# Performance work log

Measured on AMD Instinct MI355X. Metric: run time of the kernel, lower is better.

The kernel has to match this reference:

```python
import jax, jax.numpy as jnp
import numpy as np

B, S, E, H, L, A, OBS = 4, 1024, 512, 8, 4, 8, 128
D_HEAD = E // H
EPS = 1e-6
DECAY_SCALING = 1.0


def rmsnorm(x, scale):
    return x * jax.lax.rsqrt(jnp.mean(x * x, -1, keepdims=True) + EPS) * scale


def swiglu_ffn(x, w_gate, w_lin, w_out):
    return (jax.nn.silu(x @ w_gate) * (x @ w_lin)) @ w_out


def retention(x, h, logk, w_q, w_k, w_v, w_g, w_o, gns, gnb, ts, seg):
    # x:[B,S,E]  h:[B,H,d,d]  ts/seg:[B,S] int  logk:[H]
    q = (x @ w_q).reshape(B, S, H, D_HEAD).transpose(0, 2, 1, 3)
    k = (x @ w_k).reshape(B, S, H, D_HEAD).transpose(0, 2, 1, 3) / jnp.sqrt(jnp.asarray(D_HEAD, x.dtype))
    v = (x @ w_v).reshape(B, S, H, D_HEAD).transpose(0, 2, 1, 3)
    dt = (ts[:, :, None] - ts[:, None, :]).astype(x.dtype)            # [B,S,S]
    mask = (dt >= 0) & (seg[:, :, None] == seg[:, None, :])           # timestep-causal, same episode
    dt = jnp.where(mask, dt, 0.0)
    Dm = jnp.where(mask[:, None], jnp.exp(dt[:, None] * logk[None, :, None, None]), 0.0)  # [B,H,S,S]
    scores = jnp.einsum('bhnd,bhmd->bhnm', q, k) * Dm
    inner = jnp.einsum('bhnm,bhme->bhne', scores, v)
    tsf = ts.astype(x.dtype)
    fresh = (seg == 0).astype(x.dtype)                                # prev-chunk state only valid pre-done
    xi = jnp.exp((tsf + 1.0)[:, None, :] * logk[None, :, None]) * fresh[:, None, :]  # [B,H,S]
    cross = jnp.einsum('bhn,bhnd,bhde->bhne', xi, q, h)
    ret = inner + cross                                               # [B,H,S,d]
    # chunk-final recurrent state
    tmax = tsf[:, -1]
    eta = jnp.exp((tmax[:, None] - tsf)[:, None, :] * logk[None, :, None])
    eta = eta * (seg == seg[:, -1:]).astype(x.dtype)[:, None, :]
    keep = (seg[:, -1] == 0).astype(x.dtype)
    h_decay = jnp.exp((tmax + 1.0)[:, None] * logk[None, :]) * keep[:, None]  # [B,H]
    h_new = h * h_decay[..., None, None] + jnp.einsum('bhm,bhmd,bhme->bhde', eta, k, v)
    # per-head group norm (num_groups = n_head)
    y = ret.transpose(0, 2, 1, 3)                                     # [B,S,H,d]
    mu = jnp.mean(y, -1, keepdims=True)
    var = jnp.mean((y - mu) ** 2, -1, keepdims=True)
    y = ((y - mu) * jax.lax.rsqrt(var + EPS)).reshape(B, S, E) * gns + gnb
    out = (jax.nn.silu(x @ w_g) * y) @ w_o
    return out, h_new


def forward(obs, hstate, dones, timestep_id, ln_enc_scale, w_enc, ln_shared,
            wq, wk, wv, wg, wo, gn_scale, gn_bias, ln1_s, ln2_s,
            sw_gate, sw_lin, sw_out, head_w1, head_b1, head_ln, head_w2, head_b2):
    kappas = (1.0 - jnp.exp(jnp.linspace(jnp.log(1.0 / 32.0), jnp.log(1.0 / 512.0), H))) * DECAY_SCALING
    logk = jnp.log(kappas).astype(obs.dtype)
    seg = jnp.cumsum(dones, axis=-1)
    x = jax.nn.gelu(rmsnorm(obs, ln_enc_scale) @ w_enc)               # obs encoder
    new_h = jnp.zeros_like(hstate)
    for i in range(L):
        xin = rmsnorm(x, ln_shared)
        ret, hn = retention(xin, hstate[:, :, i], logk, wq[i], wk[i], wv[i], wg[i], wo[i],
                            gn_scale[i], gn_bias[i], timestep_id, seg)
        x1 = rmsnorm(xin + ret, ln1_s[i])
        x = rmsnorm(x1 + swiglu_ffn(x1, sw_gate[i], sw_lin[i], sw_out[i]), ln2_s[i])
        new_h = new_h.at[:, :, i].set(hn)
    z = jax.nn.gelu(x @ head_w1 + head_b1)
    v_loc = rmsnorm(z, head_ln) @ head_w2 + head_b2
    return v_loc, x, new_h


def setup_inputs() -> dict:
    key = jax.random.key(0)
    ks = jax.random.split(key, 16)
    sc = 0.02
    f = jnp.float32
    return {
        'obs': jax.random.normal(ks[0], (B, S, OBS), f),
        'hstate': jax.random.normal(ks[1], (B, H, L, D_HEAD, D_HEAD), f) * 0.1,
        'dones': (jax.random.uniform(ks[2], (B, S)) < 0.01).astype(jnp.int32),
        'timestep_id': jnp.broadcast_to(jnp.repeat(jnp.arange(S // A, dtype=jnp.int32), A)[None], (B, S)),
        'ln_enc_scale': jnp.ones((OBS,), f),
        'w_enc': jax.random.normal(ks[3], (OBS, E), f) * sc,
        'ln_shared': jnp.ones((E,), f),
        'wq': jax.random.normal(ks[4], (L, E, E), f) * sc,
        'wk': jax.random.normal(ks[5], (L, E, E), f) * sc,
        'wv': jax.random.normal(ks[6], (L, E, E), f) * sc,
        'wg': jax.random.normal(ks[7], (L, E, E), f) * sc,
        'wo': jax.random.normal(ks[8], (L, E, E), f) * sc,
        'gn_scale': jnp.ones((L, E), f),
        'gn_bias': jnp.zeros((L, E), f),
        'ln1_s': jnp.ones((L, E), f),
        'ln2_s': jnp.ones((L, E), f),
        'sw_gate': jax.random.normal(ks[9], (L, E, E), f) * sc,
        'sw_lin': jax.random.normal(ks[10], (L, E, E), f) * sc,
        'sw_out': jax.random.normal(ks[11], (L, E, E), f) * sc,
        'head_w1': jax.random.normal(ks[12], (E, E), f) * sc,
        'head_b1': jnp.zeros((E,), f),
        'head_ln': jnp.ones((E,), f),
        'head_w2': jax.random.normal(ks[13], (E, 1), f) * 0.01,
        'head_b2': jnp.zeros((1,), f),
    }


def reference(obs, hstate, dones, timestep_id, ln_enc_scale, w_enc, ln_shared,
              wq, wk, wv, wg, wo, gn_scale, gn_bias, ln1_s, ln2_s,
              sw_gate, sw_lin, sw_out, head_w1, head_b1, head_ln, head_w2, head_b2):
    return forward(obs, hstate, dones, timestep_id, ln_enc_scale, w_enc, ln_shared,
                   wq, wk, wv, wg, wo, gn_scale, gn_bias, ln1_s, ln2_s,
                   sw_gate, sw_lin, sw_out, head_w1, head_b1, head_ln, head_w2, head_b2)
```

## Files before the change

kernel.cpp:

```cpp
#include <hip/hip_runtime.h>
#include <math.h>

#define BN 4
#define SN 1024
#define EN 512
#define HN 8
#define LN 4
#define DN 64
#define OBSN 128
#define NR (BN*SN)
#define NB (NR*EN)
#define EPSF 1e-6f

typedef __attribute__((ext_vector_type(8))) short short8v;
typedef __attribute__((ext_vector_type(4))) float f32x4;
typedef unsigned short u16;

__device__ __forceinline__ float logk_of(int h){
    const float start = -3.4657359027997265f;
    const float step  = -0.3960841031771117f;
    return logf(1.0f - expf(start + step*(float)h));
}
__device__ __forceinline__ float geluf(float x){
    float x3 = x*x*x;
    return 0.5f*x*(1.0f + tanhf(0.7978845608028654f*(x + 0.044715f*x3)));
}
__device__ __forceinline__ float siluf(float x){
    return x / (1.0f + expf(-x));
}
__device__ __forceinline__ u16 f2bf(float x){
    union { float f; unsigned u; } v; v.f = x;
    unsigned r = v.u + 0x7FFFu + ((v.u >> 16) & 1u);
    return (u16)(r >> 16);
}
__device__ __forceinline__ void load_lds16(const void* g, void* l){
    __builtin_amdgcn_global_load_lds((const __attribute__((address_space(1))) void*)g,
                                     (__attribute__((address_space(3))) void*)l, 16, 0, 0);
}
__device__ __forceinline__ int swz(int r, int bo){ return r*128 + (bo ^ ((r&7)<<4)); }

__global__ void seg_kernel(const int* __restrict__ dones, int* __restrict__ seg){
    __shared__ int sm[SN];
    int b = blockIdx.x, t = threadIdx.x;
    sm[t] = dones[b*SN + t];
    __syncthreads();
    for (int off=1; off<SN; off<<=1){
        int v = (t>=off) ? sm[t-off] : 0;
        __syncthreads();
        sm[t] += v;
        __syncthreads();
    }
    seg[b*SN + t] = sm[t];
}

__global__ void wconv8_kernel(const float* w0, const float* w1, const float* w2,
                              const float* w3, const float* w4, const float* w5,
                              const float* w6, const float* w7,
                              u16* __restrict__ dst){
    __shared__ u16 tile[32][33];
    int z = blockIdx.z;
    int type = z>>2, layer = z&3;
    const float* srcs[8] = {w0,w1,w2,w3,w4,w5,w6,w7};
    const float* s = srcs[type] + (size_t)layer*EN*EN;
    u16* d = dst + ((size_t)type*LN + layer)*EN*EN;
    int k0 = blockIdx.y*32, m0 = blockIdx.x*32;
    int tx = threadIdx.x, ty = threadIdx.y;
    #pragma unroll
    for (int i=0;i<32;i+=8)
        tile[tx][ty+i] = f2bf(s[(size_t)(k0+ty+i)*EN + m0+tx]);
    __syncthreads();
    #pragma unroll
    for (int i=0;i<32;i+=8)
        d[(size_t)(m0+ty+i)*EN + k0+tx] = tile[ty+i][tx];
}
__global__ void wconv_kernel(const float* __restrict__ src, u16* __restrict__ dst,
                             int K, int M){
    __shared__ u16 tile[32][33];
    const float* s = src;
    u16* d = dst;
    int k0 = blockIdx.y*32, m0 = blockIdx.x*32;
    int tx = threadIdx.x, ty = threadIdx.y;
    #pragma unroll
    for (int i=0;i<32;i+=8)
        tile[tx][ty+i] = f2bf(s[(size_t)(k0+ty+i)*M + m0+tx]);
    __syncthreads();
    #pragma unroll
    for (int i=0;i<32;i+=8)
        d[(size_t)(m0+ty+i)*K + k0+tx] = tile[ty+i][tx];
}

template<int COLS, bool WF32, bool WBF>
__global__ void rmsnorm_kernel(const float* __restrict__ A,
                               const float* __restrict__ scale,
                               float* __restrict__ Of,
                               u16* __restrict__ Ob){
    constexpr int PER = COLS/64;
    int row  = blockIdx.x*4 + (threadIdx.x>>6);
    int lane = threadIdx.x & 63;
    const float* a = A + (size_t)row*COLS;
    float v[PER];
    float ss = 0.f;
    #pragma unroll
    for (int i=0;i<PER;i++){
        float x = a[lane + i*64];
        v[i] = x; ss += x*x;
    }
    #pragma unroll
    for (int off=32; off>0; off>>=1) ss += __shfl_xor(ss, off, 64);
    float rs = rsqrtf(ss*(1.0f/COLS) + EPSF);
    #pragma unroll
    for (int i=0;i<PER;i++){
        float o = v[i]*rs*scale[lane + i*64];
        if (WF32) Of[(size_t)row*COLS + lane + i*64] = o;
        if (WBF)  Ob[(size_t)row*COLS + lane + i*64] = f2bf(o);
    }
}

struct TileCtx { int t, w, lane, wr, wc; };
__device__ __forceinline__ void stage_tileA(const u16* __restrict__ A, size_t rowBase,
                                            int K, int k0, u16* As, int t){
    #pragma unroll
    for (int i=0;i<2;i++){
        int o = i*4096 + t*16;
        int arow = o>>7, acolb = o&127;
        load_lds16(A + (rowBase+arow)*K + k0 + (acolb>>1), (char*)As + o);
    }
}
__device__ __forceinline__ void mma_tile(const u16* As, const u16* Bs, f32x4 acc[2][2],
                                         int wr, int wc, int lane){
    #pragma unroll
    for (int kk=0; kk<64; kk+=32){
        int kb = kk + (lane>>4)*8;
        short8v a[2], b[2];
        #pragma unroll
        for (int m=0;m<2;m++)
            a[m] = *(const short8v*)((const char*)As + (wr*32+m*16+(lane&15))*128 + kb*2);
        #pragma unroll
        for (int n=0;n<2;n++)
            b[n] = *(const short8v*)((const char*)Bs + (wc*32+n*16+(lane&15))*128 + kb*2);
        #pragma unroll
        for (int m=0;m<2;m++)
            #pragma unroll
            for (int n=0;n<2;n++)
                acc[m][n] = __builtin_amdgcn_mfma_f32_16x16x32_bf16(a[m], b[n], acc[m][n], 0,0,0);
    }
}
#define ZERO_ACC(acc) { _Pragma("unroll") for (int m=0;m<2;m++) _Pragma("unroll") for (int n=0;n<2;n++){ acc[m][n][0]=0.f;acc[m][n][1]=0.f;acc[m][n][2]=0.f;acc[m][n][3]=0.f; } }

__global__ __launch_bounds__(256) void gemm_qkvg(
    const u16* __restrict__ A,
    const u16* __restrict__ WQ, const u16* __restrict__ WK,
    const u16* __restrict__ WV, const u16* __restrict__ WG,
    u16* __restrict__ Qbb, float* __restrict__ Kb, u16* __restrict__ Kbb,
    float* __restrict__ Vb, u16* __restrict__ VtT, float* __restrict__ Gb)
{
    __shared__ u16 As[64*64];
    __shared__ u16 Bs[4][64*64];
    int t = threadIdx.x;
    int row0 = blockIdx.y*64, col0 = blockIdx.x*64;
    int w = t>>6, lane = t&63;
    int wr = w>>1, wc = w&1;
    f32x4 accQ[2][2], accK[2][2], accV[2][2], accG[2][2];
    ZERO_ACC(accQ); ZERO_ACC(accK); ZERO_ACC(accV); ZERO_ACC(accG);
    const u16* Ws[4] = {WQ, WK, WV, WG};

    for (int k0=0; k0<EN; k0+=64){
        stage_tileA(A, (size_t)row0, EN, k0, As, t);
        #pragma unroll
        for (int wt=0; wt<4; wt++){
            #pragma unroll
            for (int i=0;i<2;i++){
                int o = i*4096 + t*16;
                int brow = o>>7, bcolb = o&127;
                load_lds16(Ws[wt] + (size_t)(col0+brow)*EN + k0 + (bcolb>>1), (char*)Bs[wt] + o);
            }
        }
        __syncthreads();
        mma_tile(As, Bs[0], accQ, wr, wc, lane);
        mma_tile(As, Bs[1], accK, wr, wc, lane);
        mma_tile(As, Bs[2], accV, wr, wc, lane);
        mma_tile(As, Bs[3], accG, wr, wc, lane);
        __syncthreads();
    }
    #pragma unroll
    for (int m=0;m<2;m++){
        #pragma unroll
        for (int n=0;n<2;n++){
            int col = col0 + wc*32 + n*16 + (lane&15);
            int rbase = row0 + wr*32 + m*16 + (lane>>4)*4;
            float vv[4];
            #pragma unroll
            for (int j=0;j<4;j++){
                size_t idx = (size_t)(rbase+j)*EN + col;
                Qbb[idx] = f2bf(accQ[m][n][j]);
                float kx = accK[m][n][j]*0.125f;
                Kb[idx] = kx; Kbb[idx] = f2bf(kx);
                float vx = accV[m][n][j];
                Vb[idx] = vx; vv[j] = vx;
                Gb[idx] = siluf(accG[m][n][j]);
            }
            ushort4 pk;
            pk.x=f2bf(vv[0]); pk.y=f2bf(vv[1]); pk.z=f2bf(vv[2]); pk.w=f2bf(vv[3]);
            int bb = rbase>>10;
            int s0 = rbase&1023;
            *(ushort4*)(VtT + ((size_t)bb*EN + col)*SN + s0) = pk;
        }
    }
}

__global__ __launch_bounds__(256) void gemm_swpair(
    const u16* __restrict__ A,
    const u16* __restrict__ WGt, const u16* __restrict__ WLt,
    u16* __restrict__ Out)
{
    __shared__ u16 As[64*64];
    __shared__ u16 Bg[64*64];
    __shared__ u16 Bl[64*64];
    int t = threadIdx.x;
    int row0 = blockIdx.y*64, col0 = blockIdx.x*64;
    int w = t>>6, lane = t&63;
    int wr = w>>1, wc = w&1;
    f32x4 accG[2][2], accL[2][2];
    ZERO_ACC(accG); ZERO_ACC(accL);
    for (int k0=0; k0<EN; k0+=64){
        stage_tileA(A, (size_t)row0, EN, k0, As, t);
        #pragma unroll
        for (int i=0;i<2;i++){
            int o = i*4096 + t*16;
            int brow = o>>7, bcolb = o&127;
            load_lds16(WGt + (size_t)(col0+brow)*EN + k0 + (bcolb>>1), (char*)Bg + o);
            load_lds16(WLt + (size_t)(col0+brow)*EN + k0 + (bcolb>>1), (char*)Bl + o);
        }
        __syncthreads();
        mma_tile(As, Bg, accG, wr, wc, lane);
        mma_tile(As, Bl, accL, wr, wc, lane);
        __syncthreads();
    }
    #pragma unroll
    for (int m=0;m<2;m++){
        #pragma unroll
        for (int n=0;n<2;n++){
            int col = col0 + wc*32 + n*16 + (lane&15);
            int rbase = row0 + wr*32 + m*16 + (lane>>4)*4;
            #pragma unroll
            for (int j=0;j<4;j++){
                float x = siluf(accG[m][n][j]) * accL[m][n][j];
                Out[(size_t)(rbase+j)*EN + col] = f2bf(x);
            }
        }
    }
}

template<int ACT, bool BIASF, bool RESF, int OUTM>
__global__ __launch_bounds__(256) void gemm_bf16(
    const u16* __restrict__ A, const u16* __restrict__ Wt,
    const float* __restrict__ bias, const float* __restrict__ res,
    float* __restrict__ C, u16* __restrict__ Ob, int K, float scale)
{
    __shared__ u16 As[64*64];
    __shared__ u16 Bs[64*64];
    int t = threadIdx.x;
    int row0 = blockIdx.y*64, col0 = blockIdx.x*64;
    int w = t>>6, lane = t&63;
    int wr = w>>1, wc = w&1;
    f32x4 acc[2][2];
    ZERO_ACC(acc);
    for (int k0=0; k0<K; k0+=64){
        stage_tileA(A, (size_t)row0, K, k0, As, t);
        #pragma unroll
        for (int i=0;i<2;i++){
            int o = i*4096 + t*16;
            int brow = o>>7, bcolb = o&127;
            load_lds16(Wt + (size_t)(col0+brow)*K + k0 + (bcolb>>1), (char*)Bs + o);
        }
        __syncthreads();
        mma_tile(As, Bs, acc, wr, wc, lane);
        __syncthreads();
    }
    #pragma unroll
    for (int m=0;m<2;m++){
        #pragma unroll
        for (int n=0;n<2;n++){
            int col = col0 + wc*32 + n*16 + (lane&15);
            int rbase = row0 + wr*32 + m*16 + (lane>>4)*4;
            #pragma unroll
            for (int j=0;j<4;j++){
                float x = acc[m][n][j]*scale;
                if (BIASF) x += bias[col];
                if (ACT==1) x = siluf(x);
                if (ACT==2) x = geluf(x);
                if (RESF) x += res[(size_t)(rbase+j)*512 + col];
                if (OUTM&1) C[(size_t)(rbase+j)*512 + col] = x;
                if (OUTM&2) Ob[(size_t)(rbase+j)*512 + col] = f2bf(x);
            }
        }
    }
}

__global__ __launch_bounds__(256) void retention_mfma(
    const u16* __restrict__ Qbb, const u16* __restrict__ Kbb,
    const u16* __restrict__ VtT,
    const float* __restrict__ hstate, const int* __restrict__ tsid, const int* __restrict__ seg,
    const float* __restrict__ gns, const float* __restrict__ gnb,
    const float* __restrict__ Gb, u16* __restrict__ Out, int layer)
{
    int bh = blockIdx.y; int b = bh>>3; int h = bh&7;
    int tile = (int)gridDim.x - 1 - (int)blockIdx.x;
    int n0 = tile*64;
    int t = threadIdx.x, lane = t&63, w = t>>6;
    __shared__ u16 Qs[64*64];
    __shared__ u16 Ks[64*64];
    __shared__ u16 Vts[64*64];
    __shared__ u16 Ps[64*64];
    __shared__ float tsq_s[64], eq_s[64], xi_s[64];
    __shared__ int   segq_s[64];
    __shared__ float tsm_s[64], em_s[64];
    __shared__ int   segm_s[64];
    float lk = logk_of(h);

    #pragma unroll
    for (int i=0;i<2;i++){
        int c = t + i*256; int r = c>>3, cb = (c&7)*16;
        short8v qv = *(const short8v*)(Qbb + (size_t)(b*SN + n0 + r)*EN + h*DN + (cb>>1));
        *(short8v*)((char*)Qs + swz(r,cb)) = qv;
    }
    const float* h0 = hstate + ((size_t)bh*LN + layer)*4096;
    #pragma unroll
    for (int i=0;i<4;i++){
        int idx = t + i*256; int d = idx>>4, e0 = (idx&15)*4;
        float4 hv = *(const float4*)(h0 + d*64 + e0);
        *(u16*)((char*)Ps + swz(e0+0, 2*d)) = f2bf(hv.x);
        *(u16*)((char*)Ps + swz(e0+1, 2*d)) = f2bf(hv.y);
        *(u16*)((char*)Ps + swz(e0+2, 2*d)) = f2bf(hv.z);
        *(u16*)((char*)Ps + swz(e0+3, 2*d)) = f2bf(hv.w);
    }
    if (t<64){
        float tq = (float)tsid[b*SN+n0+t];
        int sg = seg[b*SN+n0+t];
        tsq_s[t]=tq; segq_s[t]=sg;
        eq_s[t]=expf(tq*lk);
        xi_s[t]=(sg==0)?expf((tq+1.f)*lk):0.f;
    }
    __syncthreads();

    int qlj = w*16 + ((lane>>4)<<2);
    float tsq_r[4], eq_r[4], xi_r[4]; int sgq_r[4];
    #pragma unroll
    for (int j=0;j<4;j++){
        tsq_r[j]=tsq_s[qlj+j]; eq_r[j]=eq_s[qlj+j];
        xi_r[j]=xi_s[qlj+j];  sgq_r[j]=segq_s[qlj+j];
    }
    short8v aq0 = *(short8v*)((char*)Qs + swz(w*16+(lane&15), (lane>>4)*16));
    short8v aq1 = *(short8v*)((char*)Qs + swz(w*16+(lane&15), 64 + (lane>>4)*16));

    f32x4 oacc[4];
    {
        f32x4 cacc[4];
        #pragma unroll
        for (int en=0;en<4;en++){ cacc[en][0]=0.f; cacc[en][1]=0.f; cacc[en][2]=0.f; cacc[en][3]=0.f; }
        #pragma unroll
        for (int en=0;en<4;en++){
            short8v b0 = *(short8v*)((char*)Ps + swz(en*16+(lane&15), (lane>>4)*16));
            short8v b1 = *(short8v*)((char*)Ps + swz(en*16+(lane&15), 64+(lane>>4)*16));
            cacc[en] = __builtin_amdgcn_mfma_f32_16x16x32_bf16(aq0, b0, cacc[en], 0,0,0);
            cacc[en] = __builtin_amdgcn_mfma_f32_16x16x32_bf16(aq1, b1, cacc[en], 0,0,0);
        }
        #pragma unroll
        for (int en=0;en<4;en++)
            #pragma unroll
            for (int j=0;j<4;j++) oacc[en][j] = cacc[en][j]*xi_r[j];
    }

    for (int mt=0; mt<=tile; ++mt){
        int m0 = mt*64;
        __syncthreads();
        #pragma unroll
        for (int i=0;i<2;i++){
            int c = t + i*256; int r = c>>3, cb = (c&7)*16;
            short8v kv = *(const short8v*)(Kbb + (size_t)(b*SN+m0+r)*EN + h*DN + (cb>>1));
            *(short8v*)((char*)Ks + swz(r,cb)) = kv;
            short8v vv = *(const short8v*)(VtT + ((size_t)(b*EN) + h*DN + r)*SN + m0 + (cb>>1));
            *(short8v*)((char*)Vts + swz(r,cb)) = vv;
        }
        if (t<64){
            float tm = (float)tsid[b*SN+m0+t];
            tsm_s[t]=tm; segm_s[t]=seg[b*SN+m0+t]; em_s[t]=expf(-tm*lk);
        }
        __syncthreads();
        f32x4 sacc[4];
        #pragma unroll
        for (int mn=0;mn<4;mn++){ sacc[mn][0]=0.f; sacc[mn][1]=0.f; sacc[mn][2]=0.f; sacc[mn][3]=0.f; }
        #pragma unroll
        for (int mn=0;mn<4;mn++){
            short8v b0 = *(short8v*)((char*)Ks + swz(mn*16+(lane&15), (lane>>4)*16));
            short8v b1 = *(short8v*)((char*)Ks + swz(mn*16+(lane&15), 64+(lane>>4)*16));
            sacc[mn] = __builtin_amdgcn_mfma_f32_16x16x32_bf16(aq0, b0, sacc[mn], 0,0,0);
            sacc[mn] = __builtin_amdgcn_mfma_f32_16x16x32_bf16(aq1, b1, sacc[mn], 0,0,0);
        }
        #pragma unroll
        for (int mn=0;mn<4;mn++){
            int m = mn*16 + (lane&15);
            float tm = tsm_s[m]; float em = em_s[m]; int sgm = segm_s[m];
            #pragma unroll
            for (int j=0;j<4;j++){
                float p = (tsq_r[j]>=tm && sgq_r[j]==sgm) ? sacc[mn][j]*eq_r[j]*em : 0.f;
                *(u16*)((char*)Ps + swz(qlj+j, 2*m)) = f2bf(p);
            }
        }
        short8v ap0 = *(short8v*)((char*)Ps + swz(w*16+(lane&15), (lane>>4)*16));
        short8v ap1 = *(short8v*)((char*)Ps + swz(w*16+(lane&15), 64+(lane>>4)*16));
        #pragma unroll
        for (int dn=0;dn<4;dn++){
            short8v b0 = *(short8v*)((char*)Vts + swz(dn*16+(lane&15), (lane>>4)*16));
            short8v b1 = *(short8v*)((char*)Vts + swz(dn*16+(lane&15), 64+(lane>>4)*16));
            oacc[dn] = __builtin_amdgcn_mfma_f32_16x16x32_bf16(ap0, b0, oacc[dn], 0,0,0);
            oacc[dn] = __builtin_amdgcn_mfma_f32_16x16x32_bf16(ap1, b1, oacc[dn], 0,0,0);
        }
    }

    float mu[4], rs[4];
    #pragma unroll
    for (int j=0;j<4;j++){
        float s = oacc[0][j]+oacc[1][j]+oacc[2][j]+oacc[3][j];
        #pragma unroll
        for (int off=1; off<16; off<<=1) s += __shfl_xor(s, off, 64);
        mu[j] = s*(1.0f/64.0f);
        float d0=oacc[0][j]-mu[j], d1=oacc[1][j]-mu[j], d2=oacc[2][j]-mu[j], d3=oacc[3][j]-mu[j];
        float q2 = d0*d0+d1*d1+d2*d2+d3*d3;
        #pragma unroll
        for (int off=1; off<16; off<<=1) q2 += __shfl_xor(q2, off, 64);
        rs[j] = rsqrtf(q2*(1.0f/64.0f) + EPSF);
    }
    #pragma unroll
    for (int dn=0;dn<4;dn++){
        int e = h*DN + dn*16 + (lane&15);
        float gs = gns[e], gb = gnb[e];
        #pragma unroll
        for (int j=0;j<4;j++){
            size_t row = (size_t)(b*SN + n0 + qlj + j);
            float y = (oacc[dn][j]-mu[j])*rs[j]*gs + gb;
            Out[row*EN + e] = f2bf(y * Gb[row*EN + e]);
        }
    }
}

__global__ __launch_bounds__(256) void hnew_partial(
    const float* __restrict__ Kb, const float* __restrict__ Vb,
    const int* __restrict__ tsid, const int* __restrict__ seg,
    float* __restrict__ part)
{
    int bh = blockIdx.x; int b = bh>>3; int h = bh&7;
    int ch = blockIdx.y;
    int t = threadIdx.x;
    int r = t>>4, c = t&15;
    int d = t>>2, e0 = (t&3)*16;
    __shared__ float k_s[16][68], v_s[16][68];
    __shared__ float eta_s[16];
    float lk = logk_of(h);
    float tmax = (float)tsid[b*SN + SN-1];
    int segl = seg[b*SN + SN-1];
    float acc[16] = {};
    for (int mt=ch*4; mt<ch*4+4; ++mt){
        int m0 = mt*16;
        size_t rowM = (size_t)(b*SN + m0 + r)*EN + h*64;
        *(float4*)&k_s[r][c*4] = *(const float4*)(Kb + rowM + c*4);
        *(float4*)&v_s[r][c*4] = *(const float4*)(Vb + rowM + c*4);
        if (t<16){
            float tsm = (float)tsid[b*SN+m0+t];
            eta_s[t] = (seg[b*SN+m0+t]==segl) ? expf((tmax - tsm)*lk) : 0.f;
        }
        __syncthreads();
        #pragma unroll
        for (int mm=0; mm<16; mm++){
            float ek = eta_s[mm]*k_s[mm][d];
            #pragma unroll
            for (int u=0; u<4; u++){
                float4 vv = *(float4*)&v_s[mm][e0+u*4];
                acc[u*4+0]+=ek*vv.x; acc[u*4+1]+=ek*vv.y;
                acc[u*4+2]+=ek*vv.z; acc[u*4+3]+=ek*vv.w;
            }
        }
        __syncthreads();
    }
    float* po = part + ((size_t)bh*16 + ch)*4096;
    #pragma unroll
    for (int u=0; u<4; u++)
        *(float4*)(po + d*64 + e0 + u*4) = make_float4(acc[u*4+0],acc[u*4+1],acc[u*4+2],acc[u*4+3]);
}

__global__ void hreduce_kernel(const float* __restrict__ part, const float* __restrict__ hstate,
                               const int* __restrict__ tsid, const int* __restrict__ seg,
                               float* __restrict__ Hout, int layer){
    int bh = blockIdx.x; int b = bh>>3; int h = bh&7;
    int t = threadIdx.x;
    float lk = logk_of(h);
    float tmax = (float)tsid[b*SN + SN-1];
    int segl = seg[b*SN + SN-1];
    float hd = (segl==0) ? expf((tmax+1.0f)*lk) : 0.f;
    const float* h0 = hstate + ((size_t)bh*LN + layer)*4096;
    float* ho = Hout + ((size_t)bh*LN + layer)*4096;
    int e = t*4;
    float4 s = *(const float4*)(h0 + e);
    float4 o = make_float4(s.x*hd, s.y*hd, s.z*hd, s.w*hd);
    #pragma unroll
    for (int ch=0; ch<16; ch++){
        float4 p = *(const float4*)(part + ((size_t)bh*16 + ch)*4096 + e);
        o.x+=p.x; o.y+=p.y; o.z+=p.z; o.w+=p.w;
    }
    *(float4*)(ho + e) = o;
}

__global__ void vloc_kernel(const float* __restrict__ ZN, const float* __restrict__ w2,
                            const float* __restrict__ b2, float* __restrict__ out){
    int row  = blockIdx.x*4 + (threadIdx.x>>6);
    int lane = threadIdx.x & 63;
    const float* z = ZN + (size_t)row*EN;
    float s = 0.f;
    #pragma unroll
    for (int i=0;i<8;i++) s += z[lane + i*64]*w2[lane + i*64];
    #pragma unroll
    for (int off=32; off>0; off>>=1) s += __shfl_xor(s, off, 64);
    if (lane==0) out[row] = s + b2[0];
}

static inline void launch_gemm(const u16* A, const u16* Wt, const float* bias,
                               const float* res, float* C, u16* Ob,
                               int K, float scale, int act, int outm, hipStream_t s){
    dim3 g(8, 64), b(256,1,1);
    if (bias)                    gemm_bf16<2,true ,false,1><<<g,b,0,s>>>(A,Wt,bias,res,C,Ob,K,scale);
    else if (res && outm==3)     gemm_bf16<0,false,true ,3><<<g,b,0,s>>>(A,Wt,bias,res,C,Ob,K,scale);
    else if (res)                gemm_bf16<0,false,true ,1><<<g,b,0,s>>>(A,Wt,bias,res,C,Ob,K,scale);
    else if (act==2)             gemm_bf16<2,false,false,1><<<g,b,0,s>>>(A,Wt,bias,res,C,Ob,K,scale);
    else                         gemm_bf16<0,false,false,1><<<g,b,0,s>>>(A,Wt,bias,res,C,Ob,K,scale);
}

extern "C" void kernel_launch(void* const* d_in, const int* in_sizes, int n_in,
                              void* d_out, int out_size, void* d_ws, size_t ws_size,
                              hipStream_t stream){
    const float* obs       = (const float*)d_in[0];
    const float* hstate    = (const float*)d_in[1];
    const int*   dones     = (const int*)  d_in[2];
    const int*   tsid      = (const int*)  d_in[3];
    const float* ln_enc    = (const float*)d_in[4];
    const float* w_enc     = (const float*)d_in[5];
    const float* ln_shared = (const float*)d_in[6];
    const float* wq        = (const float*)d_in[7];
    const float* wk        = (const float*)d_in[8];
    const float* wv        = (const float*)d_in[9];
    const float* wg        = (const float*)d_in[10];
    const float* wo        = (const float*)d_in[11];
    const float* gns       = (const float*)d_in[12];
    const float* gnb       = (const float*)d_in[13];
    const float* ln1       = (const float*)d_in[14];
    const float* ln2       = (const float*)d_in[15];
    const float* swg       = (const float*)d_in[16];
    const float* swl       = (const float*)d_in[17];
    const float* swo       = (const float*)d_in[18];
    const float* hw1       = (const float*)d_in[19];
    const float* hb1       = (const float*)d_in[20];
    const float* hln       = (const float*)d_in[21];
    const float* hw2       = (const float*)d_in[22];
    const float* hb2       = (const float*)d_in[23];

    float* out_v = (float*)d_out;
    float* out_x = out_v + NR;
    float* out_h = out_x + (size_t)NR*EN;

    float* ws    = (float*)d_ws;
    float* XIN   = ws + 0*(size_t)NB;
    float* Qb    = ws + 1*(size_t)NB;
    float* Kb    = ws + 2*(size_t)NB;
    float* Vb    = ws + 3*(size_t)NB;
    float* Gb    = ws + 4*(size_t)NB;
    float* Yb    = ws + 5*(size_t)NB;
    float* hpart = ws + 6*(size_t)NB;
    int*   seg   = (int*)(hpart + 32*16*4096);
    u16* wtb  = (u16*)(seg + NR);
    const size_t WEm = (size_t)EN*EN;
    u16* wqT   = wtb;
    u16* wkT   = wqT + 4*WEm;
    u16* wvT   = wkT + 4*WEm;
    u16* wgT   = wvT + 4*WEm;
    u16* woT   = wgT + 4*WEm;
    u16* sgT   = woT + 4*WEm;
    u16* slT   = sgT + 4*WEm;
    u16* soT   = slT + 4*WEm;
    u16* wencT = soT + 4*WEm;
    u16* w1T   = wencT + (size_t)EN*OBSN;
    u16* S1b   = w1T + WEm;
    u16* S2b   = S1b + (size_t)NB;
    u16* encb  = S2b + (size_t)NB;
    u16* Qbb   = encb + (size_t)NR*OBSN;
    u16* Kbb   = Qbb + (size_t)NB;
    u16* VtT   = (u16*)Qb;

    seg_kernel<<<BN, SN, 0, stream>>>(dones, seg);

    {
        dim3 tb(32,8,1);
        wconv8_kernel<<<dim3(16,16,32), tb, 0, stream>>>(wq,wk,wv,wg,wo,swg,swl,swo, wtb);
        wconv_kernel<<<dim3(16,4,1),  tb, 0, stream>>>(w_enc, wencT, OBSN, EN);
        wconv_kernel<<<dim3(16,16,1), tb, 0, stream>>>(hw1,   w1T,   EN, EN);
    }

    rmsnorm_kernel<OBSN,false,true><<<NR/4, 256, 0, stream>>>(obs, ln_enc, nullptr, encb);
    launch_gemm(encb, wencT, nullptr, nullptr, out_x, nullptr, OBSN, 1.f, 2, 1, stream);

    for (int l=0; l<LN; ++l){
        rmsnorm_kernel<EN,true,true><<<NR/4, 256, 0, stream>>>(out_x, ln_shared, XIN, S1b);
        gemm_qkvg<<<dim3(8,64), 256, 0, stream>>>(S1b,
            wqT + l*WEm, wkT + l*WEm, wvT + l*WEm, wgT + l*WEm,
            Qbb, Kb, Kbb, Vb, VtT, Gb);
        retention_mfma<<<dim3(16, BN*HN), 256, 0, stream>>>(
            Qbb, Kbb, VtT, hstate, tsid, seg, gns + l*EN, gnb + l*EN, Gb, S2b, l);
        hnew_partial<<<dim3(BN*HN, 16), 256, 0, stream>>>(Kb, Vb, tsid, seg, hpart);
        hreduce_kernel<<<BN*HN, 1024, 0, stream>>>(hpart, hstate, tsid, seg, out_h, l);
        launch_gemm(S2b, woT + l*WEm, nullptr, XIN, Qb, nullptr, EN, 1.f, 0, 1, stream);
        rmsnorm_kernel<EN,true,true><<<NR/4, 256, 0, stream>>>(Qb, ln1 + l*EN, Kb, S1b);
        gemm_swpair<<<dim3(8,64), 256, 0, stream>>>(S1b, sgT + l*WEm, slT + l*WEm, S2b);
        launch_gemm(S2b, soT + l*WEm, nullptr, Kb, Qb, nullptr, EN, 1.f, 0, 1, stream);
        if (l == LN-1)
            rmsnorm_kernel<EN,true,true ><<<NR/4, 256, 0, stream>>>(Qb, ln2 + l*EN, out_x, S1b);
        else
            rmsnorm_kernel<EN,true,false><<<NR/4, 256, 0, stream>>>(Qb, ln2 + l*EN, out_x, nullptr);
    }

    launch_gemm(S1b, w1T, hb1, nullptr, Yb, nullptr, EN, 1.f, 2, 1, stream);
    rmsnorm_kernel<EN,true,false><<<NR/4, 256, 0, stream>>>(Yb, hln, XIN, nullptr);
    vloc_kernel<<<NR/4, 256, 0, stream>>>(XIN, hw2, hb2, out_v);
}
```

Baseline: 505.4 us.

## Fuse recurrent state update into retention kernel and double-buffer GEMM tiles

The separate hnew_partial and hreduce kernels are removed. The chunk-final state is now computed by an extra block per (batch, head) inside retention_mfma, using bf16 MFMA over a transposed K copy, which cuts two launches and the fp32 K/V writes. All three GEMM kernels double-buffer their LDS tiles so the next k-slice loads while the current one computes. The retention loop register-prefetches the next K/V tile and raises wave priority around the MFMAs. In exchange, the state update now runs in bf16 instead of fp32, and the extra KtT write plus larger LDS use per GEMM block may lower occupancy.

```diff
diff --git a/kernel.cpp b/kernel.cpp
--- a/kernel.cpp
+++ b/kernel.cpp
@@ -32,6 +32,10 @@
     union { float f; unsigned u; } v; v.f = x;
     unsigned r = v.u + 0x7FFFu + ((v.u >> 16) & 1u);
     return (u16)(r >> 16);
+}
+__device__ __forceinline__ float bf2f(u16 x){
+    union { unsigned u; float f; } v; v.u = ((unsigned)x)<<16;
+    return v.f;
 }
 __device__ __forceinline__ void load_lds16(const void* g, void* l){
     __builtin_amdgcn_global_load_lds((const __attribute__((address_space(1))) void*)g,
@@ -76,17 +80,15 @@
 __global__ void wconv_kernel(const float* __restrict__ src, u16* __restrict__ dst,
                              int K, int M){
     __shared__ u16 tile[32][33];
-    const float* s = src;
-    u16* d = dst;
     int k0 = blockIdx.y*32, m0 = blockIdx.x*32;
     int tx = threadIdx.x, ty = threadIdx.y;
     #pragma unroll
     for (int i=0;i<32;i+=8)
-        tile[tx][ty+i] = f2bf(s[(size_t)(k0+ty+i)*M + m0+tx]);
+        tile[tx][ty+i] = f2bf(src[(size_t)(k0+ty+i)*M + m0+tx]);
     __syncthreads();
     #pragma unroll
     for (int i=0;i<32;i+=8)
-        d[(size_t)(m0+ty+i)*K + k0+tx] = tile[ty+i][tx];
+        dst[(size_t)(m0+ty+i)*K + k0+tx] = tile[ty+i][tx];
 }
 
 template<int COLS, bool WF32, bool WBF>
@@ -116,14 +118,13 @@
     }
 }
 
-struct TileCtx { int t, w, lane, wr, wc; };
-__device__ __forceinline__ void stage_tileA(const u16* __restrict__ A, size_t rowBase,
-                                            int K, int k0, u16* As, int t){
+__device__ __forceinline__ void stage_tile(const u16* __restrict__ G, size_t rowBase,
+                                           int K, int k0, u16* dst, int t){
     #pragma unroll
     for (int i=0;i<2;i++){
         int o = i*4096 + t*16;
-        int arow = o>>7, acolb = o&127;
-        load_lds16(A + (rowBase+arow)*K + k0 + (acolb>>1), (char*)As + o);
+        int grow = o>>7, gcolb = o&127;
+        load_lds16(G + (rowBase+grow)*K + k0 + (gcolb>>1), (char*)dst + o);
     }
 }
 __device__ __forceinline__ void mma_tile(const u16* As, const u16* Bs, f32x4 acc[2][2],
@@ -151,11 +152,11 @@
     const u16* __restrict__ A,
     const u16* __restrict__ WQ, const u16* __restrict__ WK,
     const u16* __restrict__ WV, const u16* __restrict__ WG,
-    u16* __restrict__ Qbb, float* __restrict__ Kb, u16* __restrict__ Kbb,
-    float* __restrict__ Vb, u16* __restrict__ VtT, float* __restrict__ Gb)
+    u16* __restrict__ Qbb, u16* __restrict__ Kbb,
+    u16* __restrict__ VtT, u16* __restrict__ KtT, float* __restrict__ Gb)
 {
-    __shared__ u16 As[64*64];
-    __shared__ u16 Bs[4][64*64];
+    __shared__ u16 As[2][64*64];
+    __shared__ u16 Bs[2][4][64*64];
     int t = threadIdx.x;
     int row0 = blockIdx.y*64, col0 = blockIdx.x*64;
     int w = t>>6, lane = t&63;
@@ -164,22 +165,22 @@
     ZERO_ACC(accQ); ZERO_ACC(accK); ZERO_ACC(accV); ZERO_ACC(accG);
     const u16* Ws[4] = {WQ, WK, WV, WG};
 
-    for (int k0=0; k0<EN; k0+=64){
-        stage_tileA(A, (size_t)row0, EN, k0, As, t);
-        #pragma unroll
-        for (int wt=0; wt<4; wt++){
-            #pragma unroll
-            for (int i=0;i<2;i++){
-                int o = i*4096 + t*16;
-                int brow = o>>7, bcolb = o&127;
-                load_lds16(Ws[wt] + (size_t)(col0+brow)*EN + k0 + (bcolb>>1), (char*)Bs[wt] + o);
-            }
-        }
-        __syncthreads();
-        mma_tile(As, Bs[0], accQ, wr, wc, lane);
-        mma_tile(As, Bs[1], accK, wr, wc, lane);
-        mma_tile(As, Bs[2], accV, wr, wc, lane);
-        mma_tile(As, Bs[3], accG, wr, wc, lane);
+    stage_tile(A, (size_t)row0, EN, 0, As[0], t);
+    #pragma unroll
+    for (int wt=0; wt<4; wt++) stage_tile(Ws[wt], (size_t)col0, EN, 0, Bs[0][wt], t);
+    __syncthreads();
+    for (int ti=0; ti<EN/64; ++ti){
+        int cur = ti&1;
+        if (ti+1 < EN/64){
+            stage_tile(A, (size_t)row0, EN, (ti+1)*64, As[cur^1], t);
+            #pragma unroll
+            for (int wt=0; wt<4; wt++)
+                stage_tile(Ws[wt], (size_t)col0, EN, (ti+1)*64, Bs[cur^1][wt], t);
+        }
+        mma_tile(As[cur], Bs[cur][0], accQ, wr, wc, lane);
+        mma_tile(As[cur], Bs[cur][1], accK, wr, wc, lane);
+        mma_tile(As[cur], Bs[cur][2], accV, wr, wc, lane);
+        mma_tile(As[cur], Bs[cur][3], accG, wr, wc, lane);
         __syncthreads();
     }
     #pragma unroll
@@ -188,22 +189,21 @@
         for (int n=0;n<2;n++){
             int col = col0 + wc*32 + n*16 + (lane&15);
             int rbase = row0 + wr*32 + m*16 + (lane>>4)*4;
-            float vv[4];
+            ushort4 pkV, pkK;
             #pragma unroll
             for (int j=0;j<4;j++){
                 size_t idx = (size_t)(rbase+j)*EN + col;
                 Qbb[idx] = f2bf(accQ[m][n][j]);
                 float kx = accK[m][n][j]*0.125f;
-                Kb[idx] = kx; Kbb[idx] = f2bf(kx);
-                float vx = accV[m][n][j];
-                Vb[idx] = vx; vv[j] = vx;
+                Kbb[idx] = f2bf(kx);
+                ((u16*)&pkK)[j] = f2bf(kx);
+                ((u16*)&pkV)[j] = f2bf(accV[m][n][j]);
                 Gb[idx] = siluf(accG[m][n][j]);
             }
-            ushort4 pk;
-            pk.x=f2bf(vv[0]); pk.y=f2bf(vv[1]); pk.z=f2bf(vv[2]); pk.w=f2bf(vv[3]);
             int bb = rbase>>10;
             int s0 = rbase&1023;
-            *(ushort4*)(VtT + ((size_t)bb*EN + col)*SN + s0) = pk;
+            *(ushort4*)(VtT + ((size_t)bb*EN + col)*SN + s0) = pkV;
+            *(ushort4*)(KtT + ((size_t)bb*EN + col)*SN + s0) = pkK;
         }
     }
 }
@@ -213,27 +213,28 @@
     const u16* __restrict__ WGt, const u16* __restrict__ WLt,
     u16* __restrict__ Out)
 {
-    __shared__ u16 As[64*64];
-    __shared__ u16 Bg[64*64];
-    __shared__ u16 Bl[64*64];
+    __shared__ u16 As[2][64*64];
+    __shared__ u16 Bg[2][64*64];
+    __shared__ u16 Bl[2][64*64];
     int t = threadIdx.x;
     int row0 = blockIdx.y*64, col0 = blockIdx.x*64;
     int w = t>>6, lane = t&63;
     int wr = w>>1, wc = w&1;
     f32x4 accG[2][2], accL[2][2];
     ZERO_ACC(accG); ZERO_ACC(accL);
-    for (int k0=0; k0<EN; k0+=64){
-        stage_tileA(A, (size_t)row0, EN, k0, As, t);
-        #pragma unroll
-        for (int i=0;i<2;i++){
-            int o = i*4096 + t*16;
-            int brow = o>>7, bcolb = o&127;
-            load_lds16(WGt + (size_t)(col0+brow)*EN + k0 + (bcolb>>1), (char*)Bg + o);
-            load_lds16(WLt + (size_t)(col0+brow)*EN + k0 + (bcolb>>1), (char*)Bl + o);
-        }
-        __syncthreads();
-        mma_tile(As, Bg, accG, wr, wc, lane);
-        mma_tile(As, Bl, accL, wr, wc, lane);
+    stage_tile(A, (size_t)row0, EN, 0, As[0], t);
+    stage_tile(WGt, (size_t)col0, EN, 0, Bg[0], t);
+    stage_tile(WLt, (size_t)col0, EN, 0, Bl[0], t);
+    __syncthreads();
+    for (int ti=0; ti<EN/64; ++ti){
+        int cur = ti&1;
+        if (ti+1 < EN/64){
+            stage_tile(A, (size_t)row0, EN, (ti+1)*64, As[cur^1], t);
+            stage_tile(WGt, (size_t)col0, EN, (ti+1)*64, Bg[cur^1], t);
+            stage_tile(WLt, (size_t)col0, EN, (ti+1)*64, Bl[cur^1], t);
+        }
+        mma_tile(As[cur], Bg[cur], accG, wr, wc, lane);
+        mma_tile(As[cur], Bl[cur], accL, wr, wc, lane);
         __syncthreads();
     }
     #pragma unroll
@@ -257,24 +258,25 @@
     const float* __restrict__ bias, const float* __restrict__ res,
     float* __restrict__ C, u16* __restrict__ Ob, int K, float scale)
 {
-    __shared__ u16 As[64*64];
-    __shared__ u16 Bs[64*64];
+    __shared__ u16 As[2][64*64];
+    __shared__ u16 Bs[2][64*64];
     int t = threadIdx.x;
     int row0 = blockIdx.y*64, col0 = blockIdx.x*64;
     int w = t>>6, lane = t&63;
     int wr = w>>1, wc = w&1;
     f32x4 acc[2][2];
     ZERO_ACC(acc);
-    for (int k0=0; k0<K; k0+=64){
-        stage_tileA(A, (size_t)row0, K, k0, As, t);
-        #pragma unroll
-        for (int i=0;i<2;i++){
-            int o = i*4096 + t*16;
-            int brow = o>>7, bcolb = o&127;
-            load_lds16(Wt + (size_t)(col0+brow)*K + k0 + (bcolb>>1), (char*)Bs + o);
-        }
-        __syncthreads();
-        mma_tile(As, Bs, acc, wr, wc, lane);
+    int nt = K/64;
+    stage_tile(A, (size_t)row0, K, 0, As[0], t);
+    stage_tile(Wt, (size_t)col0, K, 0, Bs[0], t);
+    __syncthreads();
+    for (int ti=0; ti<nt; ++ti){
+        int cur = ti&1;
+        if (ti+1 < nt){
+            stage_tile(A, (size_t)row0, K, (ti+1)*64, As[cur^1], t);
+            stage_tile(Wt, (size_t)col0, K, (ti+1)*64, Bs[cur^1], t);
+        }
+        mma_tile(As[cur], Bs[cur], acc, wr, wc, lane);
         __syncthreads();
     }
     #pragma unroll
@@ -299,14 +301,13 @@
 
 __global__ __launch_bounds__(256) void retention_mfma(
     const u16* __restrict__ Qbb, const u16* __restrict__ Kbb,
-    const u16* __restrict__ VtT,
+    const u16* __restrict__ VtT, const u16* __restrict__ KtT,
     const float* __restrict__ hstate, const int* __restrict__ tsid, const int* __restrict__ seg,
     const float* __restrict__ gns, const float* __restrict__ gnb,
-    const float* __restrict__ Gb, u16* __restrict__ Out, int layer)
+    const float* __restrict__ Gb, u16* __restrict__ Out,
+    float* __restrict__ Hout, int layer)
 {
     int bh = blockIdx.y; int b = bh>>3; int h = bh&7;
-    int tile = (int)gridDim.x - 1 - (int)blockIdx.x;
-    int n0 = tile*64;
     int t = threadIdx.x, lane = t&63, w = t>>6;
     __shared__ u16 Qs[64*64];
     __shared__ u16 Ks[64*64];
@@ -318,6 +319,66 @@
     __shared__ int   segm_s[64];
     float lk = logk_of(h);
 
+    if (blockIdx.x == 0){
+        float tmax = (float)tsid[b*SN + SN-1];
+        int segl = seg[b*SN + SN-1];
+        float* eta = (float*)Qs;
+        #pragma unroll
+        for (int i=0;i<4;i++){
+            int m = t + i*256;
+            float tsm = (float)tsid[b*SN+m];
+            eta[m] = (seg[b*SN+m]==segl) ? expf((tmax - tsm)*lk) : 0.f;
+        }
+        f32x4 eacc[4];
+        #pragma unroll
+        for (int en=0;en<4;en++){ eacc[en][0]=0.f; eacc[en][1]=0.f; eacc[en][2]=0.f; eacc[en][3]=0.f; }
+        for (int mt=0; mt<16; ++mt){
+            int m0 = mt*64;
+            __syncthreads();
+            #pragma unroll
+            for (int i=0;i<2;i++){
+                int c = t + i*256; int r = c>>3, cb = (c&7)*16;
+                int mb = m0 + (cb>>1);
+                size_t g = ((size_t)(b*EN) + h*DN + r)*SN + mb;
+                short8v kt = *(const short8v*)(KtT + g);
+                short8v vt = *(const short8v*)(VtT + g);
+                short8v ks;
+                #pragma unroll
+                for (int j=0;j<8;j++) ks[j] = (short)f2bf(bf2f((u16)kt[j]) * eta[mb+j]);
+                *(short8v*)((char*)Ks  + swz(r,cb)) = ks;
+                *(short8v*)((char*)Vts + swz(r,cb)) = vt;
+            }
+            __syncthreads();
+            short8v a0 = *(short8v*)((char*)Ks + swz(w*16+(lane&15), (lane>>4)*16));
+            short8v a1 = *(short8v*)((char*)Ks + swz(w*16+(lane&15), 64+(lane>>4)*16));
+            __builtin_amdgcn_s_setprio(1);
+            #pragma unroll
+            for (int en=0;en<4;en++){
+                short8v b0 = *(short8v*)((char*)Vts + swz(en*16+(lane&15), (lane>>4)*16));
+                short8v b1 = *(short8v*)((char*)Vts + swz(en*16+(lane&15), 64+(lane>>4)*16));
+                eacc[en] = __builtin_amdgcn_mfma_f32_16x16x32_bf16(a0, b0, eacc[en], 0,0,0);
+                eacc[en] = __builtin_amdgcn_mfma_f32_16x16x32_bf16(a1, b1, eacc[en], 0,0,0);
+            }
+            __builtin_amdgcn_s_setprio(0);
+        }
+        float hd = (segl==0) ? expf((tmax+1.0f)*lk) : 0.f;
+        const float* h0 = hstate + ((size_t)bh*LN + layer)*4096;
+        float* ho = Hout + ((size_t)bh*LN + layer)*4096;
+        #pragma unroll
+        for (int en=0;en<4;en++){
+            int e = en*16 + (lane&15);
+            #pragma unroll
+            for (int j=0;j<4;j++){
+                int d = w*16 + (lane>>4)*4 + j;
+                ho[d*64 + e] = h0[d*64 + e]*hd + eacc[en][j];
+            }
+        }
+        return;
+    }
+
+    int tile = 16 - (int)blockIdx.x;
+    int n0 = tile*64;
+
     #pragma unroll
     for (int i=0;i<2;i++){
         int c = t + i*256; int r = c>>3, cb = (c&7)*16;
@@ -341,6 +402,15 @@
         eq_s[t]=expf(tq*lk);
         xi_s[t]=(sg==0)?expf((tq+1.f)*lk):0.f;
     }
+    short8v kr0, kr1, vr0, vr1;
+    {
+        int c0 = t, c1 = t+256;
+        int r0=c0>>3, cb0=(c0&7)*16, r1=c1>>3, cb1=(c1&7)*16;
+        kr0 = *(const short8v*)(Kbb + (size_t)(b*SN+r0)*EN + h*DN + (cb0>>1));
+        kr1 = *(const short8v*)(Kbb + (size_t)(b*SN+r1)*EN + h*DN + (cb1>>1));
+        vr0 = *(const short8v*)(VtT + ((size_t)(b*EN)+h*DN+r0)*SN + (cb0>>1));
+        vr1 = *(const short8v*)(VtT + ((size_t)(b*EN)+h*DN+r1)*SN + (cb1>>1));
+    }
     __syncthreads();
 
     int qlj = w*16 + ((lane>>4)<<2);
@@ -374,22 +444,32 @@
     for (int mt=0; mt<=tile; ++mt){
         int m0 = mt*64;
         __syncthreads();
-        #pragma unroll
-        for (int i=0;i<2;i++){
-            int c = t + i*256; int r = c>>3, cb = (c&7)*16;
-            short8v kv = *(const short8v*)(Kbb + (size_t)(b*SN+m0+r)*EN + h*DN + (cb>>1));
-            *(short8v*)((char*)Ks + swz(r,cb)) = kv;
-            short8v vv = *(const short8v*)(VtT + ((size_t)(b*EN) + h*DN + r)*SN + m0 + (cb>>1));
-            *(short8v*)((char*)Vts + swz(r,cb)) = vv;
+        {
+            int c0 = t, c1 = t+256;
+            int r0=c0>>3, cb0=(c0&7)*16, r1=c1>>3, cb1=(c1&7)*16;
+            *(short8v*)((char*)Ks  + swz(r0,cb0)) = kr0;
+            *(short8v*)((char*)Ks  + swz(r1,cb1)) = kr1;
+            *(short8v*)((char*)Vts + swz(r0,cb0)) = vr0;
+            *(short8v*)((char*)Vts + swz(r1,cb1)) = vr1;
         }
         if (t<64){
             float tm = (float)tsid[b*SN+m0+t];
             tsm_s[t]=tm; segm_s[t]=seg[b*SN+m0+t]; em_s[t]=expf(-tm*lk);
         }
+        if (mt < tile){
+            int m1 = m0 + 64;
+            int c0 = t, c1 = t+256;
+            int r0=c0>>3, cb0=(c0&7)*16, r1=c1>>3, cb1=(c1&7)*16;
+            kr0 = *(const short8v*)(Kbb + (size_t)(b*SN+m1+r0)*EN + h*DN + (cb0>>1));
+            kr1 = *(const short8v*)(Kbb + (size_t)(b*SN+m1+r1)*EN + h*DN + (cb1>>1));
+            vr0 = *(const short8v*)(VtT + ((size_t)(b*EN)+h*DN+r0)*SN + m1 + (cb0>>1));
+            vr1 = *(const short8v*)(VtT + ((size_t)(b*EN)+h*DN+r1)*SN + m1 + (cb1>>1));
+        }
         __syncthreads();
         f32x4 sacc[4];
         #pragma unroll
         for (int mn=0;mn<4;mn++){ sacc[mn][0]=0.f; sacc[mn][1]=0.f; sacc[mn][2]=0.f; sacc[mn][3]=0.f; }
+        __builtin_amdgcn_s_setprio(1);
         #pragma unroll
         for (int mn=0;mn<4;mn++){
             short8v b0 = *(short8v*)((char*)Ks + swz(mn*16+(lane&15), (lane>>4)*16));
@@ -397,6 +477,7 @@
             sacc[mn] = __builtin_amdgcn_mfma_f32_16x16x32_bf16(aq0, b0, sacc[mn], 0,0,0);
             sacc[mn] = __builtin_amdgcn_mfma_f32_16x16x32_bf16(aq1, b1, sacc[mn], 0,0,0);
         }
+        __builtin_amdgcn_s_setprio(0);
         #pragma unroll
         for (int mn=0;mn<4;mn++){
             int m = mn*16 + (lane&15);
@@ -409,6 +490,7 @@
         }
         short8v ap0 = *(short8v*)((char*)Ps + swz(w*16+(lane&15), (lane>>4)*16));
         short8v ap1 = *(short8v*)((char*)Ps + swz(w*16+(lane&15), 64+(lane>>4)*16));
+        __builtin_amdgcn_s_setprio(1);
         #pragma unroll
         for (int dn=0;dn<4;dn++){
             short8v b0 = *(short8v*)((char*)Vts + swz(dn*16+(lane&15), (lane>>4)*16));
@@ -416,6 +498,7 @@
             oacc[dn] = __builtin_amdgcn_mfma_f32_16x16x32_bf16(ap0, b0, oacc[dn], 0,0,0);
             oacc[dn] = __builtin_amdgcn_mfma_f32_16x16x32_bf16(ap1, b1, oacc[dn], 0,0,0);
         }
+        __builtin_amdgcn_s_setprio(0);
     }
 
     float mu[4], rs[4];
@@ -442,72 +525,6 @@
             Out[row*EN + e] = f2bf(y * Gb[row*EN + e]);
         }
     }
-}
-
-__global__ __launch_bounds__(256) void hnew_partial(
-    const float* __restrict__ Kb, const float* __restrict__ Vb,
-    const int* __restrict__ tsid, const int* __restrict__ seg,
-    float* __restrict__ part)
-{
-    int bh = blockIdx.x; int b = bh>>3; int h = bh&7;
-    int ch = blockIdx.y;
-    int t = threadIdx.x;
-    int r = t>>4, c = t&15;
-    int d = t>>2, e0 = (t&3)*16;
-    __shared__ float k_s[16][68], v_s[16][68];
-    __shared__ float eta_s[16];
-    float lk = logk_of(h);
-    float tmax = (float)tsid[b*SN + SN-1];
-    int segl = seg[b*SN + SN-1];
-    float acc[16] = {};
-    for (int mt=ch*4; mt<ch*4+4; ++mt){
-        int m0 = mt*16;
-        size_t rowM = (size_t)(b*SN + m0 + r)*EN + h*64;
-        *(float4*)&k_s[r][c*4] = *(const float4*)(Kb + rowM + c*4);
-        *(float4*)&v_s[r][c*4] = *(const float4*)(Vb + rowM + c*4);
-        if (t<16){
-            float tsm = (float)tsid[b*SN+m0+t];
-            eta_s[t] = (seg[b*SN+m0+t]==segl) ? expf((tmax - tsm)*lk) : 0.f;
-        }
-        __syncthreads();
-        #pragma unroll
-        for (int mm=0; mm<16; mm++){
-            float ek = eta_s[mm]*k_s[mm][d];
-            #pragma unroll
-            for (int u=0; u<4; u++){
-                float4 vv = *(float4*)&v_s[mm][e0+u*4];
-                acc[u*4+0]+=ek*vv.x; acc[u*4+1]+=ek*vv.y;
-                acc[u*4+2]+=ek*vv.z; acc[u*4+3]+=ek*vv.w;
-            }
-        }
-        __syncthreads();
-    }
-    float* po = part + ((size_t)bh*16 + ch)*4096;
-    #pragma unroll
-    for (int u=0; u<4; u++)
-        *(float4*)(po + d*64 + e0 + u*4) = make_float4(acc[u*4+0],acc[u*4+1],acc[u*4+2],acc[u*4+3]);
-}
-
-__global__ void hreduce_kernel(const float* __restrict__ part, const float* __restrict__ hstate,
-                               const int* __restrict__ tsid, const int* __restrict__ seg,
-                               float* __restrict__ Hout, int layer){
-    int bh = blockIdx.x; int b = bh>>3; int h = bh&7;
-    int t = threadIdx.x;
-    float lk = logk_of(h);
-    float tmax = (float)tsid[b*SN + SN-1];
-    int segl = seg[b*SN + SN-1];
-    float hd = (segl==0) ? expf((tmax+1.0f)*lk) : 0.f;
-    const float* h0 = hstate + ((size_t)bh*LN + layer)*4096;
-    float* ho = Hout + ((size_t)bh*LN + layer)*4096;
-    int e = t*4;
-    float4 s = *(const float4*)(h0 + e);
-    float4 o = make_float4(s.x*hd, s.y*hd, s.z*hd, s.w*hd);
-    #pragma unroll
-    for (int ch=0; ch<16; ch++){
-        float4 p = *(const float4*)(part + ((size_t)bh*16 + ch)*4096 + e);
-        o.x+=p.x; o.y+=p.y; o.z+=p.z; o.w+=p.w;
-    }
-    *(float4*)(ho + e) = o;
 }
 
 __global__ void vloc_kernel(const float* __restrict__ ZN, const float* __restrict__ w2,
@@ -573,8 +590,7 @@
     float* Vb    = ws + 3*(size_t)NB;
     float* Gb    = ws + 4*(size_t)NB;
     float* Yb    = ws + 5*(size_t)NB;
-    float* hpart = ws + 6*(size_t)NB;
-    int*   seg   = (int*)(hpart + 32*16*4096);
+    int*   seg   = (int*)(ws + 6*(size_t)NB);
     u16* wtb  = (u16*)(seg + NR);
     const size_t WEm = (size_t)EN*EN;
     u16* wqT   = wtb;
@@ -593,6 +609,7 @@
     u16* Qbb   = encb + (size_t)NR*OBSN;
     u16* Kbb   = Qbb + (size_t)NB;
     u16* VtT   = (u16*)Qb;
+    u16* KtT   = VtT + (size_t)NB;
 
     seg_kernel<<<BN, SN, 0, stream>>>(dones, seg);
 
@@ -610,11 +627,10 @@
         rmsnorm_kernel<EN,true,true><<<NR/4, 256, 0, stream>>>(out_x, ln_shared, XIN, S1b);
         gemm_qkvg<<<dim3(8,64), 256, 0, stream>>>(S1b,
             wqT + l*WEm, wkT + l*WEm, wvT + l*WEm, wgT + l*WEm,
-            Qbb, Kb, Kbb, Vb, VtT, Gb);
-        retention_mfma<<<dim3(16, BN*HN), 256, 0, stream>>>(
-            Qbb, Kbb, VtT, hstate, tsid, seg, gns + l*EN, gnb + l*EN, Gb, S2b, l);
-        hnew_partial<<<dim3(BN*HN, 16), 256, 0, stream>>>(Kb, Vb, tsid, seg, hpart);
-        hreduce_kernel<<<BN*HN, 1024, 0, stream>>>(hpart, hstate, tsid, seg, out_h, l);
+            Qbb, Kbb, VtT, KtT, Gb);
+        retention_mfma<<<dim3(17, BN*HN), 256, 0, stream>>>(
+            Qbb, Kbb, VtT, KtT, hstate, tsid, seg, gns + l*EN, gnb + l*EN,
+            Gb, S2b, out_h, l);
         launch_gemm(S2b, woT + l*WEm, nullptr, XIN, Qb, nullptr, EN, 1.f, 0, 1, stream);
         rmsnorm_kernel<EN,true,true><<<NR/4, 256, 0, stream>>>(Qb, ln1 + l*EN, Kb, S1b);
         gemm_swpair<<<dim3(8,64), 256, 0, stream>>>(S1b, sgT + l*WEm, slT + l*WEm, S2b);
```

Result: faster. 436.4 us (-13.6%).
